# Kernel optimization log

Measured on AMD Instinct MI355X. Metric: run time of the kernel, lower is better.

The kernel has to match this reference:

```python
import jax, jax.numpy as jnp
import numpy as np

B, SZ_C, S, D_KV, H_DIM = 2048, 8, 32, 32, 512
NEG = B // 4  # batchsize > 64 branch
TEMP = 0.5
EPS = 1e-8
BN_EPS = 1e-5


def setup_inputs() -> dict:
    key = jax.random.key(0)
    ks = jax.random.split(key, 8)
    x = jax.random.normal(ks[0], (B, SZ_C, S, D_KV), dtype=jnp.float32)
    W1 = jax.random.normal(ks[1], (H_DIM, D_KV), dtype=jnp.float32) * 0.05
    b1 = jnp.zeros((H_DIM,), jnp.float32)
    gamma = jnp.ones((H_DIM,), jnp.float32)
    beta = jnp.zeros((H_DIM,), jnp.float32)
    W2 = jax.random.normal(ks[2], (D_KV, H_DIM), dtype=jnp.float32) * 0.05
    b2 = jnp.zeros((D_KV,), jnp.float32)
    fcW = jax.random.normal(ks[3], (32, S * D_KV), dtype=jnp.float32) * 0.03
    fcb = jnp.zeros((32,), jnp.float32)
    # negatives: raw draws in [0, B-1); shifted past the self index inside reference
    neg_idx = jax.random.randint(ks[4], (B, NEG), 0, B - 1, dtype=jnp.int32)
    return {"x": x, "W1": W1, "b1": b1, "gamma": gamma, "beta": beta,
            "W2": W2, "b2": b2, "fcW": fcW, "fcb": fcb, "neg_idx": neg_idx}


def reference(x, W1, b1, gamma, beta, W2, b2, fcW, fcb, neg_idx):
    # per-channel MLP with training-mode BatchNorm (stats over the B*S rows of each channel)
    xc = jnp.transpose(x, (1, 0, 2, 3)).reshape(SZ_C, B * S, D_KV)   # [C, N, d_kv]
    h = jnp.einsum('cnd,hd->cnh', xc, W1) + b1                        # [C, N, h]
    mu = jnp.mean(h, axis=1, keepdims=True)
    var = jnp.mean((h - mu) ** 2, axis=1, keepdims=True)              # biased, as BN
    h = jax.nn.relu((h - mu) * jax.lax.rsqrt(var + BN_EPS) * gamma + beta)
    y = jnp.einsum('cnh,dh->cnd', h, W2) + b2                         # [C, N, d_kv]
    y = y.reshape(SZ_C, B, S * D_KV)                                  # raw flatten == torch views
    Zc = jnp.einsum('cbf,of->cbo', y, fcW) + fcb                      # [C, B, 32]
    Z = jnp.transpose(Zc, (1, 0, 2))                                  # [B, C, 32]

    Zn = Z / jnp.clip(jnp.linalg.norm(Z, axis=-1, keepdims=True), EPS, None)

    # shift raw draws in [0, B-1) past i -> uniform over indices != i
    idx = neg_idx + (neg_idx >= jnp.arange(B, dtype=neg_idx.dtype)[:, None]).astype(neg_idx.dtype)
    neg = Zn[idx]                                                     # [B, NEG, C, 32]
    neg_sim = jnp.einsum('bcd,bncd->bn', Zn, neg) / SZ_C              # mean over channels

    # mean pairwise cosine similarity across channels (j < k)
    G = jnp.einsum('bjd,bkd->bjk', Zn, Zn)                            # [B, C, C]
    mask = jnp.triu(jnp.ones((SZ_C, SZ_C), bool), 1)
    num_comb = SZ_C * (SZ_C - 1) // 2
    pos_sim = jnp.where(mask, G, 0.0).sum(axis=(1, 2)) / num_comb     # [B]

    l = jnp.exp(pos_sim / TEMP) / jnp.sum(jnp.exp(neg_sim / TEMP), axis=1)  # [B]
    Z_out = jnp.mean(Z, axis=1)                                       # [B, 32]
    return Z_out, l
```

## Files before the change

### kernel.cpp

```cpp
#include <hip/hip_runtime.h>
#include <hip/hip_bf16.h>
#include <math.h>

#define NB 2048
#define NC 8
#define NNEG 512

typedef __attribute__((ext_vector_type(8))) short bf16x8;
typedef __attribute__((ext_vector_type(4))) float f32x4;
typedef __attribute__((ext_vector_type(16))) float f32x16;

static __device__ __forceinline__ unsigned short f2b(float f) {
  __hip_bfloat16 h = __float2bfloat16(f);
  return *reinterpret_cast<unsigned short*>(&h);
}
static __device__ __forceinline__ unsigned int pack_rn(float a, float b) {
  unsigned int ua = __float_as_uint(a) + 0x8000u;
  unsigned int ub = __float_as_uint(b) + 0x8000u;
  return __builtin_amdgcn_perm(ub, ua, 0x07060302u);
}

#define WS_SSUM   0
#define WS_SPROD  256
#define WS_B1EFF  8448
#define WS_Z      12544
#define WS_POS    536832
#define WS_W1B    538880
#define WS_W2B    604416
#define WS_FCWB   612608
#define WS_ZNB    628992

__global__ __launch_bounds__(256) void k_stats(const float* __restrict__ x,
                        float* __restrict__ Ssum, float* __restrict__ Sprod) {
  int c = blockIdx.y;
  int t = threadIdx.x;
  int w = t >> 6, l = t & 63;
  int col = l & 31, half = l >> 5;
  f32x16 acc;
  #pragma unroll
  for (int r = 0; r < 16; ++r) acc[r] = 0.f;
  float ssum = 0.f;
  #pragma unroll 2
  for (int i = 0; i < 8; ++i) {
    int chunk = blockIdx.x * 32 + i * 4 + w;
    int b = chunk >> 1;
    int sb = (chunk & 1) * 16 + half * 8;
    const float* base = x + ((size_t)(b * NC + c)) * 1024 + sb * 32 + col;
    float v0 = base[0],   v1 = base[32],  v2 = base[64],  v3 = base[96];
    float v4 = base[128], v5 = base[160], v6 = base[192], v7 = base[224];
    ssum += ((v0 + v1) + (v2 + v3)) + ((v4 + v5) + (v6 + v7));
    uint4 fq;
    fq.x = pack_rn(v0, v1); fq.y = pack_rn(v2, v3);
    fq.z = pack_rn(v4, v5); fq.w = pack_rn(v6, v7);
    bf16x8 f = __builtin_bit_cast(bf16x8, fq);
    acc = __builtin_amdgcn_mfma_f32_32x32x16_bf16(f, f, acc, 0, 0, 0);
  }
  __shared__ float pr[4][1024];
  __shared__ float sred[4][32];
  #pragma unroll
  for (int r = 0; r < 16; ++r) {
    int row = (r & 3) + 8 * (r >> 2) + 4 * half;
    pr[w][row * 32 + col] = acc[r];
  }
  float sv = ssum + __shfl_xor(ssum, 32);
  if (l < 32) sred[w][l] = sv;
  __syncthreads();
  #pragma unroll
  for (int p = 0; p < 4; ++p) {
    int cell = t + p * 256;
    atomicAdd(&Sprod[c * 1024 + cell],
              (pr[0][cell] + pr[1][cell]) + (pr[2][cell] + pr[3][cell]));
  }
  if (t < 32)
    atomicAdd(&Ssum[c * 32 + t],
              (sred[0][t] + sred[1][t]) + (sred[2][t] + sred[3][t]));
}

__global__ void k_foldcvt(const float* __restrict__ W1, const float* __restrict__ b1,
                       const float* __restrict__ gamma, const float* __restrict__ beta,
                       const float* __restrict__ Ssum, const float* __restrict__ Sprod,
                       const float* __restrict__ W2, const float* __restrict__ fcW,
                       unsigned short* __restrict__ W1B, float* __restrict__ b1eff,
                       unsigned short* __restrict__ W2B, unsigned short* __restrict__ fcWB) {
  if (blockIdx.x >= 16) {
    int j = (blockIdx.x - 16) * 256 + threadIdx.x;
    if (j < 8192)
      ((unsigned int*)W2B)[j] = pack_rn(W2[2 * j], W2[2 * j + 1]);
    ((unsigned int*)fcWB)[j] = pack_rn(fcW[2 * j], fcW[2 * j + 1]);
    return;
  }
  int g = blockIdx.x * 256 + threadIdx.x;
  int c = g >> 9, h = g & 511;
  const float invN = 1.0f / (float)(NB * 32);
  float w[32];
  #pragma unroll
  for (int d = 0; d < 32; ++d) w[d] = W1[h * 32 + d];
  const float* M = Sprod + c * 1024;
  float q = 0.f;
  for (int j = 0; j < 32; ++j) {
    float v = 0.f;
    #pragma unroll
    for (int i2 = 0; i2 < 32; ++i2) v = fmaf(w[i2], M[i2 * 32 + j], v);
    q = fmaf(v, w[j], q);
  }
  float wmu = 0.f;
  #pragma unroll
  for (int d = 0; d < 32; ++d) wmu = fmaf(w[d], Ssum[c * 32 + d] * invN, wmu);
  float bb = b1[h];
  float mean = wmu + bb;
  float e2 = q * invN + 2.f * bb * wmu + bb * bb;
  float var = e2 - mean * mean;
  float alpha = gamma[h] * rsqrtf(var + 1e-5f);
  unsigned int* W1Bu = (unsigned int*)&W1B[((size_t)c * 512 + h) * 32];
  #pragma unroll
  for (int d = 0; d < 16; ++d)
    W1Bu[d] = pack_rn(w[2 * d] * alpha, w[2 * d + 1] * alpha);
  b1eff[c * 512 + h] = (bb - mean) * alpha + beta[h];
}

__global__ __launch_bounds__(256, 3) void k_main(
    const float* __restrict__ x, const unsigned short* __restrict__ W1B,
    const float* __restrict__ b1eff, const unsigned short* __restrict__ W2B,
    const float* __restrict__ b2, const unsigned short* __restrict__ fcWB,
    const float* __restrict__ fcb, float* __restrict__ Z) {
  int c = blockIdx.y;
  int bt = blockIdx.x;
  int t = threadIdx.x;
  int w = t >> 6, l = t & 63;
  int lr = l & 15, lg = l >> 4;

  __shared__ unsigned int rbuf[4][64][20];
  __shared__ float zred[2][8][32];

  const unsigned short* W1c = W1B + (size_t)c * 512 * 32;
  const float* b1e = b1eff + c * 512;
  unsigned int* rbw = &rbuf[w][0][0];

  bf16x8 xf[4];
  #pragma unroll
  for (int sb = 0; sb < 4; ++sb) {
    int bl = 2 * w + (sb >> 1);
    int s = (sb & 1) * 16 + lr;
    const float* src = x + (((size_t)(bt * 8 + bl) * NC + c) * 32 + s) * 32 + lg * 8;
    float4 v0 = ((const float4*)src)[0];
    float4 v1 = ((const float4*)src)[1];
    uint4 fq;
    fq.x = pack_rn(v0.x, v0.y); fq.y = pack_rn(v0.z, v0.w);
    fq.z = pack_rn(v1.x, v1.y); fq.w = pack_rn(v1.z, v1.w);
    xf[sb] = __builtin_bit_cast(bf16x8, fq);
  }

  f32x4 yacc[4][2];
  #pragma unroll
  for (int db = 0; db < 2; ++db) {
    f32x4 bv = *((const f32x4*)(b2 + db * 16 + lg * 4));
    #pragma unroll
    for (int mb = 0; mb < 4; ++mb) yacc[mb][db] = bv;
  }

  bf16x8 wfR[2];   f32x4 biasR[2];   bf16x8 w2fR[2];   bf16x8 hfreg[4];
  wfR[0]  = *(const bf16x8*)&W1c[(size_t)lr * 32 + lg * 8];
  wfR[1]  = *(const bf16x8*)&W1c[(size_t)(16 + lr) * 32 + lg * 8];
  biasR[0] = *(const f32x4*)(b1e + lg * 4);
  biasR[1] = *(const f32x4*)(b1e + 16 + lg * 4);

#define GEMM1(dfr) \
  _Pragma("unroll") for (int hb = 0; hb < 2; ++hb) \
  _Pragma("unroll") for (int sb = 0; sb < 4; ++sb) \
    dfr[hb][sb] = __builtin_amdgcn_mfma_f32_16x16x32_bf16(wfR[hb], xf[sb], biasR[hb], 0, 0, 0);

#define GEMM2() \
  _Pragma("unroll") for (int mb = 0; mb < 4; ++mb) { \
    yacc[mb][0] = __builtin_amdgcn_mfma_f32_16x16x32_bf16(w2fR[0], hfreg[mb], yacc[mb][0], 0, 0, 0); \
    yacc[mb][1] = __builtin_amdgcn_mfma_f32_16x16x32_bf16(w2fR[1], hfreg[mb], yacc[mb][1], 0, 0, 0); \
  }

#define PACKWRITE(dfr) \
  _Pragma("unroll") for (int hb = 0; hb < 2; ++hb) \
  _Pragma("unroll") for (int sb = 0; sb < 4; ++sb) { \
    uint2 pk; \
    pk.x = pack_rn(fmaxf(dfr[hb][sb][0], 0.f), fmaxf(dfr[hb][sb][1], 0.f)); \
    pk.y = pack_rn(fmaxf(dfr[hb][sb][2], 0.f), fmaxf(dfr[hb][sb][3], 0.f)); \
    *(uint2*)&rbw[(sb * 16 + lr) * 20 + hb * 8 + lg * 2] = pk; \
  }

#define LOADW(ch) { \
    if ((ch) < 15) { \
      int h1 = ((ch) + 1) * 32; \
      wfR[0]  = *(const bf16x8*)&W1c[(size_t)(h1 + lr) * 32 + lg * 8]; \
      wfR[1]  = *(const bf16x8*)&W1c[(size_t)(h1 + 16 + lr) * 32 + lg * 8]; \
      biasR[0] = *(const f32x4*)(b1e + h1 + lg * 4); \
      biasR[1] = *(const f32x4*)(b1e + h1 + 16 + lg * 4); \
    } \
    w2fR[0] = *(const bf16x8*)&W2B[(size_t)lr * 512 + (ch) * 32 + lg * 8]; \
    w2fR[1] = *(const bf16x8*)&W2B[(size_t)(16 + lr) * 512 + (ch) * 32 + lg * 8]; \
  }

#define READH() \
  _Pragma("unroll") for (int mb = 0; mb < 4; ++mb) \
    hfreg[mb] = *(const bf16x8*)&rbw[(mb * 16 + lr) * 20 + lg * 4];

  {
    f32x4 dfr[2][4];
    GEMM1(dfr);
    PACKWRITE(dfr);
    LOADW(0);
    READH();
  }
  #pragma unroll 3
  for (int ch = 1; ch < 16; ++ch) {
    f32x4 dfr[2][4];
    GEMM1(dfr);
    GEMM2();
    PACKWRITE(dfr);
    LOADW(ch);
    READH();
  }
  GEMM2();

  #pragma unroll
  for (int mb = 0; mb < 4; ++mb) {
    #pragma unroll
    for (int db = 0; db < 2; ++db) {
      uint2 pk;
      pk.x = pack_rn(yacc[mb][db][0], yacc[mb][db][1]);
      pk.y = pack_rn(yacc[mb][db][2], yacc[mb][db][3]);
      *(uint2*)&rbw[(mb * 16 + lr) * 20 + db * 8 + lg * 2] = pk;
    }
  }
  __syncthreads();

  int nt = w & 1, kh = w >> 1;
  int arow = (lr < 8) ? lr : 7;
  const unsigned int* ybase = &rbuf[arow >> 1][(arow & 1) * 32][0];
  f32x4 zacc = {0.f, 0.f, 0.f, 0.f};
  #pragma unroll
  for (int ks = 0; ks < 16; ++ks) {
    int s = kh * 16 + ks;
    uint4 av = *(const uint4*)&ybase[s * 20 + lg * 4];
    bf16x8 afc = __builtin_bit_cast(bf16x8, av);
    bf16x8 bfc = *(const bf16x8*)&fcWB[(size_t)(nt * 16 + lr) * 1024 + s * 32 + lg * 8];
    zacc = __builtin_amdgcn_mfma_f32_16x16x32_bf16(afc, bfc, zacc, 0, 0, 0);
  }
  if (lg < 2) {
    #pragma unroll
    for (int r = 0; r < 4; ++r) zred[kh][lg * 4 + r][nt * 16 + lr] = zacc[r];
  }
  __syncthreads();
  {
    int bloc = t >> 5, o = t & 31;
    Z[((size_t)(bt * 8 + bloc) * NC + c) * 32 + o] =
        zred[0][bloc][o] + zred[1][bloc][o] + fcb[o];
  }
#undef GEMM1
#undef GEMM2
#undef PACKWRITE
#undef LOADW
#undef READH
}

__global__ void k_znorm(const float* __restrict__ Z, unsigned short* __restrict__ Znb,
                        float* __restrict__ possim, float* __restrict__ out) {
  int b = blockIdx.x;
  int t = threadIdx.x;
  float v = Z[(size_t)b * 256 + t];
  float n2 = v * v;
  #pragma unroll
  for (int m = 16; m >= 1; m >>= 1) n2 += __shfl_xor(n2, m, 64);
  float nrm = fmaxf(sqrtf(n2), 1e-8f);
  float zn = v / nrm;
  Znb[(size_t)b * 256 + t] = f2b(zn);
  __shared__ float sz[256];
  __shared__ float szn[256];
  sz[t] = v; szn[t] = zn;
  __syncthreads();
  if (t < 32) {
    float s = 0.f;
    #pragma unroll
    for (int cc = 0; cc < 8; ++cc) s += sz[cc * 32 + t];
    out[(size_t)b * 32 + t] = s * 0.125f;
    float sd = 0.f, t1 = 0.f;
    #pragma unroll
    for (int cc = 0; cc < 8; ++cc) {
      float z2 = szn[cc * 32 + t];
      sd += z2; t1 = fmaf(z2, z2, t1);
    }
    float t2 = sd * sd;
    #pragma unroll
    for (int m = 16; m >= 1; m >>= 1) {
      t2 += __shfl_xor(t2, m, 64);
      t1 += __shfl_xor(t1, m, 64);
    }
    if (t == 0) possim[b] = (t2 - t1) * 0.5f / 28.0f;
  }
}

__global__ __launch_bounds__(256) void k_negsim(
    const unsigned short* __restrict__ Znb, const int* __restrict__ neg_idx,
    const float* __restrict__ possim, float* __restrict__ lout) {
  int b = blockIdx.x;
  int t = threadIdx.x;
  int w = t >> 6, l = t & 63;
  int lr = l & 15, lg = l >> 4;
  __shared__ uint4 selfv[32];
  __shared__ float rs[4];
  if (t < 32) selfv[t] = ((const uint4*)(Znb + (size_t)b * 256))[t];
  __syncthreads();
  const unsigned short* selfp = (const unsigned short*)selfv;
  const f32x4 fzero = {0.f, 0.f, 0.f, 0.f};
  float esum = 0.f;
  #pragma unroll 2
  for (int mb = 0; mb < 8; ++mb) {
    int m0 = w * 128 + mb * 16;
    int raw = neg_idx[(size_t)b * NNEG + m0 + lr];
    int j = raw + (raw >= b ? 1 : 0);
    const unsigned short* rp = Znb + (size_t)j * 256;
    f32x4 acc = fzero;
    #pragma unroll
    for (int ks = 0; ks < 8; ++ks) {
      bf16x8 af = *(const bf16x8*)(rp + ks * 32 + lg * 8);
      bf16x8 bf = *(const bf16x8*)(selfp + ks * 32 + lg * 8);
      acc = __builtin_amdgcn_mfma_f32_16x16x32_bf16(af, bf, acc, 0, 0, 0);
    }
    if (lr == 0) {
      esum += expf(acc[0] * 0.25f) + expf(acc[1] * 0.25f)
            + expf(acc[2] * 0.25f) + expf(acc[3] * 0.25f);
    }
  }
  #pragma unroll
  for (int m = 32; m >= 1; m >>= 1) esum += __shfl_xor(esum, m, 64);
  if (l == 0) rs[w] = esum;
  __syncthreads();
  if (t == 0) {
    float tot = rs[0] + rs[1] + rs[2] + rs[3];
    lout[b] = expf(possim[b] * 2.0f) / tot;
  }
}

extern "C" void kernel_launch(void* const* d_in, const int* in_sizes, int n_in,
                              void* d_out, int out_size, void* d_ws, size_t ws_size,
                              hipStream_t stream) {
  const float* x     = (const float*)d_in[0];
  const float* W1    = (const float*)d_in[1];
  const float* b1    = (const float*)d_in[2];
  const float* gamma = (const float*)d_in[3];
  const float* beta  = (const float*)d_in[4];
  const float* W2    = (const float*)d_in[5];
  const float* b2    = (const float*)d_in[6];
  const float* fcW   = (const float*)d_in[7];
  const float* fcb   = (const float*)d_in[8];
  const int*   nidx  = (const int*)d_in[9];
  float* ws = (float*)d_ws;
  float* Ssum   = ws + WS_SSUM;
  float* Sprod  = ws + WS_SPROD;
  float* b1eff  = ws + WS_B1EFF;
  float* Z      = ws + WS_Z;
  float* possim = ws + WS_POS;
  unsigned short* W1Bp  = (unsigned short*)(ws + WS_W1B);
  unsigned short* W2Bp  = (unsigned short*)(ws + WS_W2B);
  unsigned short* fcWBp = (unsigned short*)(ws + WS_FCWB);
  unsigned short* Znbp  = (unsigned short*)(ws + WS_ZNB);
  float* out = (float*)d_out;

  hipMemsetAsync(ws, 0, (256 + 8192) * sizeof(float), stream);
  k_stats<<<dim3(128, 8), 256, 0, stream>>>(x, Ssum, Sprod);
  k_foldcvt<<<80, 256, 0, stream>>>(W1, b1, gamma, beta, Ssum, Sprod, W2, fcW,
                                    W1Bp, b1eff, W2Bp, fcWBp);
  k_main<<<dim3(256, 8), 256, 0, stream>>>(x, W1Bp, b1eff, W2Bp, b2, fcWBp, fcb, Z);
  k_znorm<<<NB, 256, 0, stream>>>(Z, Znbp, possim, out);
  k_negsim<<<NB, 256, 0, stream>>>(Znbp, nidx, possim, out + NB * 32);
}
```

Before: 180.4 us.

## Make k_main persistent over four batch tiles with prefetched x loads

Each k_main block now processes four consecutive batch tiles instead of one, cutting the grid from 256x8 to 64x8 blocks. The x fragments for the next tile are loaded and converted to bf16 during the tail of the current tile, overlapping global loads with the fc epilogue. Occupancy hint drops from 3 to 2 blocks per SIMD to leave room for the extra prefetch registers. The cost is fewer blocks (512 total) on a chip with many CUs, so parallelism is lower and the load may be imbalanced.

```diff
diff --git a/kernel.cpp b/kernel.cpp
--- a/kernel.cpp
+++ b/kernel.cpp
@@ -19,6 +19,7 @@
   unsigned int ub = __float_as_uint(b) + 0x8000u;
   return __builtin_amdgcn_perm(ub, ua, 0x07060302u);
 }
+#define MF16(a, b, c) __builtin_amdgcn_mfma_f32_16x16x32_bf16((a), (b), (c), 0, 0, 0)
 
 #define WS_SSUM   0
 #define WS_SPROD  256
@@ -118,13 +119,13 @@
   b1eff[c * 512 + h] = (bb - mean) * alpha + beta[h];
 }
 
-__global__ __launch_bounds__(256, 3) void k_main(
+__global__ __launch_bounds__(256, 2) void k_main(
     const float* __restrict__ x, const unsigned short* __restrict__ W1B,
     const float* __restrict__ b1eff, const unsigned short* __restrict__ W2B,
     const float* __restrict__ b2, const unsigned short* __restrict__ fcWB,
     const float* __restrict__ fcb, float* __restrict__ Z) {
   int c = blockIdx.y;
-  int bt = blockIdx.x;
+  int bt0 = blockIdx.x * 4;
   int t = threadIdx.x;
   int w = t >> 6, l = t & 63;
   int lr = l & 15, lg = l >> 4;
@@ -136,43 +137,37 @@
   const float* b1e = b1eff + c * 512;
   unsigned int* rbw = &rbuf[w][0][0];
 
-  bf16x8 xf[4];
-  #pragma unroll
-  for (int sb = 0; sb < 4; ++sb) {
-    int bl = 2 * w + (sb >> 1);
-    int s = (sb & 1) * 16 + lr;
-    const float* src = x + (((size_t)(bt * 8 + bl) * NC + c) * 32 + s) * 32 + lg * 8;
-    float4 v0 = ((const float4*)src)[0];
-    float4 v1 = ((const float4*)src)[1];
-    uint4 fq;
-    fq.x = pack_rn(v0.x, v0.y); fq.y = pack_rn(v0.z, v0.w);
-    fq.z = pack_rn(v1.x, v1.y); fq.w = pack_rn(v1.z, v1.w);
-    xf[sb] = __builtin_bit_cast(bf16x8, fq);
-  }
-
-  f32x4 yacc[4][2];
-  #pragma unroll
-  for (int db = 0; db < 2; ++db) {
-    f32x4 bv = *((const f32x4*)(b2 + db * 16 + lg * 4));
-    #pragma unroll
-    for (int mb = 0; mb < 4; ++mb) yacc[mb][db] = bv;
-  }
-
   bf16x8 wfR[2];   f32x4 biasR[2];   bf16x8 w2fR[2];   bf16x8 hfreg[4];
-  wfR[0]  = *(const bf16x8*)&W1c[(size_t)lr * 32 + lg * 8];
-  wfR[1]  = *(const bf16x8*)&W1c[(size_t)(16 + lr) * 32 + lg * 8];
-  biasR[0] = *(const f32x4*)(b1e + lg * 4);
-  biasR[1] = *(const f32x4*)(b1e + 16 + lg * 4);
+  bf16x8 xf[4], xfN[4];
+
+#define LOADX(dst, bti) \
+  _Pragma("unroll") for (int sb = 0; sb < 4; ++sb) { \
+    int bl = 2 * w + (sb >> 1); \
+    int s = (sb & 1) * 16 + lr; \
+    const float* src = x + (((size_t)((bti) * 8 + bl) * NC + c) * 32 + s) * 32 + lg * 8; \
+    float4 v0 = ((const float4*)src)[0]; \
+    float4 v1 = ((const float4*)src)[1]; \
+    uint4 fq; \
+    fq.x = pack_rn(v0.x, v0.y); fq.y = pack_rn(v0.z, v0.w); \
+    fq.z = pack_rn(v1.x, v1.y); fq.w = pack_rn(v1.z, v1.w); \
+    dst[sb] = __builtin_bit_cast(bf16x8, fq); \
+  }
+
+#define LDWF0() { \
+    wfR[0]  = *(const bf16x8*)&W1c[(size_t)lr * 32 + lg * 8]; \
+    wfR[1]  = *(const bf16x8*)&W1c[(size_t)(16 + lr) * 32 + lg * 8]; \
+    biasR[0] = *(const f32x4*)(b1e + lg * 4); \
+    biasR[1] = *(const f32x4*)(b1e + 16 + lg * 4); }
 
 #define GEMM1(dfr) \
   _Pragma("unroll") for (int hb = 0; hb < 2; ++hb) \
   _Pragma("unroll") for (int sb = 0; sb < 4; ++sb) \
-    dfr[hb][sb] = __builtin_amdgcn_mfma_f32_16x16x32_bf16(wfR[hb], xf[sb], biasR[hb], 0, 0, 0);
+    dfr[hb][sb] = MF16(wfR[hb], xf[sb], biasR[hb]);
 
 #define GEMM2() \
   _Pragma("unroll") for (int mb = 0; mb < 4; ++mb) { \
-    yacc[mb][0] = __builtin_amdgcn_mfma_f32_16x16x32_bf16(w2fR[0], hfreg[mb], yacc[mb][0], 0, 0, 0); \
-    yacc[mb][1] = __builtin_amdgcn_mfma_f32_16x16x32_bf16(w2fR[1], hfreg[mb], yacc[mb][1], 0, 0, 0); \
+    yacc[mb][0] = MF16(w2fR[0], hfreg[mb], yacc[mb][0]); \
+    yacc[mb][1] = MF16(w2fR[1], hfreg[mb], yacc[mb][1]); \
   }
 
 #define PACKWRITE(dfr) \
@@ -200,58 +195,84 @@
   _Pragma("unroll") for (int mb = 0; mb < 4; ++mb) \
     hfreg[mb] = *(const bf16x8*)&rbw[(mb * 16 + lr) * 20 + lg * 4];
 
-  {
-    f32x4 dfr[2][4];
-    GEMM1(dfr);
-    PACKWRITE(dfr);
-    LOADW(0);
-    READH();
-  }
-  #pragma unroll 3
-  for (int ch = 1; ch < 16; ++ch) {
-    f32x4 dfr[2][4];
-    GEMM1(dfr);
+  LOADX(xf, bt0);
+  LDWF0();
+
+  for (int tt = 0; tt < 4; ++tt) {
+    int bt = bt0 + tt;
+
+    f32x4 yacc[4][2];
+    #pragma unroll
+    for (int db = 0; db < 2; ++db) {
+      f32x4 bv = *((const f32x4*)(b2 + db * 16 + lg * 4));
+      #pragma unroll
+      for (int mb = 0; mb < 4; ++mb) yacc[mb][db] = bv;
+    }
+
+    {
+      f32x4 dfr[2][4];
+      GEMM1(dfr);
+      PACKWRITE(dfr);
+      LOADW(0);
+      READH();
+    }
+    #pragma unroll 3
+    for (int ch = 1; ch < 16; ++ch) {
+      f32x4 dfr[2][4];
+      GEMM1(dfr);
+      GEMM2();
+      PACKWRITE(dfr);
+      LOADW(ch);
+      READH();
+    }
     GEMM2();
-    PACKWRITE(dfr);
-    LOADW(ch);
-    READH();
-  }
-  GEMM2();
-
-  #pragma unroll
-  for (int mb = 0; mb < 4; ++mb) {
-    #pragma unroll
-    for (int db = 0; db < 2; ++db) {
-      uint2 pk;
-      pk.x = pack_rn(yacc[mb][db][0], yacc[mb][db][1]);
-      pk.y = pack_rn(yacc[mb][db][2], yacc[mb][db][3]);
-      *(uint2*)&rbw[(mb * 16 + lr) * 20 + db * 8 + lg * 2] = pk;
-    }
-  }
-  __syncthreads();
-
-  int nt = w & 1, kh = w >> 1;
-  int arow = (lr < 8) ? lr : 7;
-  const unsigned int* ybase = &rbuf[arow >> 1][(arow & 1) * 32][0];
-  f32x4 zacc = {0.f, 0.f, 0.f, 0.f};
-  #pragma unroll
-  for (int ks = 0; ks < 16; ++ks) {
-    int s = kh * 16 + ks;
-    uint4 av = *(const uint4*)&ybase[s * 20 + lg * 4];
-    bf16x8 afc = __builtin_bit_cast(bf16x8, av);
-    bf16x8 bfc = *(const bf16x8*)&fcWB[(size_t)(nt * 16 + lr) * 1024 + s * 32 + lg * 8];
-    zacc = __builtin_amdgcn_mfma_f32_16x16x32_bf16(afc, bfc, zacc, 0, 0, 0);
-  }
-  if (lg < 2) {
-    #pragma unroll
-    for (int r = 0; r < 4; ++r) zred[kh][lg * 4 + r][nt * 16 + lr] = zacc[r];
-  }
-  __syncthreads();
-  {
-    int bloc = t >> 5, o = t & 31;
-    Z[((size_t)(bt * 8 + bloc) * NC + c) * 32 + o] =
-        zred[0][bloc][o] + zred[1][bloc][o] + fcb[o];
-  }
+
+    if (tt < 3) LOADX(xfN, bt + 1);
+    LDWF0();
+
+    #pragma unroll
+    for (int mb = 0; mb < 4; ++mb) {
+      #pragma unroll
+      for (int db = 0; db < 2; ++db) {
+        uint2 pk;
+        pk.x = pack_rn(yacc[mb][db][0], yacc[mb][db][1]);
+        pk.y = pack_rn(yacc[mb][db][2], yacc[mb][db][3]);
+        *(uint2*)&rbw[(mb * 16 + lr) * 20 + db * 8 + lg * 2] = pk;
+      }
+    }
+    __syncthreads();
+
+    {
+      int nt = w & 1, kh = w >> 1;
+      int arow = (lr < 8) ? lr : 7;
+      const unsigned int* ybase = &rbuf[arow >> 1][(arow & 1) * 32][0];
+      f32x4 zacc = {0.f, 0.f, 0.f, 0.f};
+      #pragma unroll
+      for (int ks = 0; ks < 16; ++ks) {
+        int s = kh * 16 + ks;
+        uint4 av = *(const uint4*)&ybase[s * 20 + lg * 4];
+        bf16x8 afc = __builtin_bit_cast(bf16x8, av);
+        bf16x8 bfc = *(const bf16x8*)&fcWB[(size_t)(nt * 16 + lr) * 1024 + s * 32 + lg * 8];
+        zacc = MF16(afc, bfc, zacc);
+      }
+      if (lg < 2) {
+        #pragma unroll
+        for (int r = 0; r < 4; ++r) zred[kh][lg * 4 + r][nt * 16 + lr] = zacc[r];
+      }
+    }
+    __syncthreads();
+    {
+      int bloc = t >> 5, o = t & 31;
+      Z[((size_t)(bt * 8 + bloc) * NC + c) * 32 + o] =
+          zred[0][bloc][o] + zred[1][bloc][o] + fcb[o];
+    }
+    if (tt < 3) {
+      #pragma unroll
+      for (int sb = 0; sb < 4; ++sb) xf[sb] = xfN[sb];
+    }
+  }
+#undef LOADX
+#undef LDWF0
 #undef GEMM1
 #undef GEMM2
 #undef PACKWRITE
@@ -320,7 +341,7 @@
     for (int ks = 0; ks < 8; ++ks) {
       bf16x8 af = *(const bf16x8*)(rp + ks * 32 + lg * 8);
       bf16x8 bf = *(const bf16x8*)(selfp + ks * 32 + lg * 8);
-      acc = __builtin_amdgcn_mfma_f32_16x16x32_bf16(af, bf, acc, 0, 0, 0);
+      acc = MF16(af, bf, acc);
     }
     if (lr == 0) {
       esum += expf(acc[0] * 0.25f) + expf(acc[1] * 0.25f)
@@ -366,7 +387,7 @@
   k_stats<<<dim3(128, 8), 256, 0, stream>>>(x, Ssum, Sprod);
   k_foldcvt<<<80, 256, 0, stream>>>(W1, b1, gamma, beta, Ssum, Sprod, W2, fcW,
                                     W1Bp, b1eff, W2Bp, fcWBp);
-  k_main<<<dim3(256, 8), 256, 0, stream>>>(x, W1Bp, b1eff, W2Bp, b2, fcWBp, fcb, Z);
+  k_main<<<dim3(64, 8), 256, 0, stream>>>(x, W1Bp, b1eff, W2Bp, b2, fcWBp, fcb, Z);
   k_znorm<<<NB, 256, 0, stream>>>(Z, Znbp, possim, out);
   k_negsim<<<NB, 256, 0, stream>>>(Znbp, nidx, possim, out + NB * 32);
 }
```

Result: faster. 176.9 us (-2.0%).
